# Kernel optimization log

Hardware: AMD Instinct MI355X
Metric: run time of the kernel (lower is better)

Reference implementation:

```python
import jax, jax.numpy as jnp
import numpy as np

B, K, D = 128, 32, 1024
E = 32
H = int(D * 0.25)  # d_hidden = d_block * moe_ratio


def _rsqrt_uniform(key, shape, d):
    bound = d ** -0.5
    return jax.random.uniform(key, shape, jnp.float32, -bound, bound)


def setup_inputs() -> dict:
    key = jax.random.key(0)
    ks = jax.random.split(key, 7)
    return {
        "x": jax.random.normal(ks[0], (B, K, D), jnp.float32),
        "router_w": _rsqrt_uniform(ks[1], (E, D), D),   # nn.Linear(d_block, num_experts).weight
        "router_b": _rsqrt_uniform(ks[2], (E,), D),
        "weights1": _rsqrt_uniform(ks[3], (E, D, H), H),
        "bias1": _rsqrt_uniform(ks[4], (E, H), H),
        "weights2": _rsqrt_uniform(ks[5], (E, H, D), D),
        "bias2": _rsqrt_uniform(ks[6], (E, D), D),
    }


def reference(x, router_w, router_b, weights1, bias1, weights2, bias2):
    b, k, d = x.shape
    x_flat = x.reshape(-1, d)                      # [N, D], N = B*K
    n = x_flat.shape[0]
    # top-1 router (argmax of logits, like torch.argmax)
    logits = x_flat @ router_w.T + router_b        # [N, E]
    routed_idx = jnp.argmax(logits, axis=-1)       # [N]

    # Each expert is a 2-layer MLP; note the original applies act1 (ReLU)
    # after BOTH layers, and dropout=0.0 is an identity.
    def expert_mlp(w1, b1, w2, b2):
        h = jax.nn.relu(x_flat @ w1 + b1)          # [N, H]
        return jax.nn.relu(h @ w2 + b2)            # [N, D]

    y_all = jax.vmap(expert_mlp)(weights1, bias1, weights2, bias2)  # [E, N, D]
    out_flat = y_all[routed_idx, jnp.arange(n)]    # select routed expert per token
    return out_flat.reshape(b, k, d)
```

## Files before the change

kernel.cpp:

```cpp
#include <hip/hip_runtime.h>


#define N_TOK 4096
#define DDIM  1024
#define HDIM  256
#define NEXP  32
#define TPX   136
#define NSLOT (8 * TPX)

typedef __attribute__((ext_vector_type(8))) short bf16x8;
typedef __attribute__((ext_vector_type(4))) float f32x4;

__device__ __forceinline__ unsigned short f2bf(float f) {
  union { float f; unsigned u; } v; v.f = f;
  unsigned r = v.u + 0x7FFFu + ((v.u >> 16) & 1u);
  return (unsigned short)(r >> 16);
}
__device__ __forceinline__ float bf2f(unsigned short h) {
  union { unsigned u; float f; } v; v.u = ((unsigned)h) << 16;
  return v.f;
}
__device__ __forceinline__ int swz(int row, int kk) {
  return row * 72 + (kk ^ (((row >> 3) & 7) << 3));
}

__global__ __launch_bounds__(512) void router_kernel(
    const float* __restrict__ x, const float* __restrict__ rw,
    const float* __restrict__ rb, int* __restrict__ routed) {
  __shared__ float red[8][64][8];
  int b = blockIdx.x;
  int t = threadIdx.x, w = t >> 6, l = t & 63;
  int m = l & 15, kb = l >> 4;
  int tok = b * 16 + m;
  int kbase = w * 128;
  bf16x8 wh[2][4], wl[2][4];
#pragma unroll
  for (int h = 0; h < 2; h++) {
    const float* wp = rw + (size_t)(m + h * 16) * DDIM + kbase + kb * 8;
#pragma unroll
    for (int q = 0; q < 4; q++) {
      float4 f0 = *(const float4*)(wp + q * 32);
      float4 f1 = *(const float4*)(wp + q * 32 + 4);
      float fv[8] = {f0.x, f0.y, f0.z, f0.w, f1.x, f1.y, f1.z, f1.w};
      bf16x8 hi, lo;
#pragma unroll
      for (int i = 0; i < 8; i++) {
        unsigned short hh = f2bf(fv[i]);
        hi[i] = (short)hh;
        lo[i] = (short)f2bf(fv[i] - bf2f(hh));
      }
      wh[h][q] = hi; wl[h][q] = lo;
    }
  }
  const float* xrow = x + (size_t)tok * DDIM + kbase + kb * 8;
  f32x4 acc0 = {0.f,0.f,0.f,0.f}, acc1 = {0.f,0.f,0.f,0.f};
#pragma unroll
  for (int q = 0; q < 4; q++) {
    float4 xa = *(const float4*)(xrow + q * 32);
    float4 xc = *(const float4*)(xrow + q * 32 + 4);
    float xv[8] = {xa.x, xa.y, xa.z, xa.w, xc.x, xc.y, xc.z, xc.w};
    bf16x8 xhi, xlo;
#pragma unroll
    for (int i = 0; i < 8; i++) {
      unsigned short hh = f2bf(xv[i]);
      xhi[i] = (short)hh;
      xlo[i] = (short)f2bf(xv[i] - bf2f(hh));
    }
    acc0 = __builtin_amdgcn_mfma_f32_16x16x32_bf16(xhi, wh[0][q], acc0, 0, 0, 0);
    acc0 = __builtin_amdgcn_mfma_f32_16x16x32_bf16(xlo, wh[0][q], acc0, 0, 0, 0);
    acc0 = __builtin_amdgcn_mfma_f32_16x16x32_bf16(xhi, wl[0][q], acc0, 0, 0, 0);
    acc0 = __builtin_amdgcn_mfma_f32_16x16x32_bf16(xlo, wl[0][q], acc0, 0, 0, 0);
    acc1 = __builtin_amdgcn_mfma_f32_16x16x32_bf16(xhi, wh[1][q], acc1, 0, 0, 0);
    acc1 = __builtin_amdgcn_mfma_f32_16x16x32_bf16(xlo, wh[1][q], acc1, 0, 0, 0);
    acc1 = __builtin_amdgcn_mfma_f32_16x16x32_bf16(xhi, wl[1][q], acc1, 0, 0, 0);
    acc1 = __builtin_amdgcn_mfma_f32_16x16x32_bf16(xlo, wl[1][q], acc1, 0, 0, 0);
  }
  *(f32x4*)&red[w][l][0] = acc0;
  *(f32x4*)&red[w][l][4] = acc1;
  __syncthreads();
  if (w == 0) {
    f32x4 s0 = {0.f,0.f,0.f,0.f}, s1 = {0.f,0.f,0.f,0.f};
#pragma unroll
    for (int ww = 0; ww < 8; ww++) {
      s0 += *(const f32x4*)&red[ww][l][0];
      s1 += *(const f32x4*)&red[ww][l][4];
    }
    float rb0 = rb[m], rb1 = rb[16 + m];
#pragma unroll
    for (int r = 0; r < 4; r++) {
      float v0 = s0[r] + rb0;
      float v1 = s1[r] + rb1;
      float val = v0; int idx = m;
      if (v1 > v0) { val = v1; idx = 16 + m; }
#pragma unroll
      for (int s = 1; s < 16; s <<= 1) {
        float ov = __shfl_xor(val, s);
        int oi = __shfl_xor(idx, s);
        if (ov > val || (ov == val && oi < idx)) { val = ov; idx = oi; }
      }
      if (m == 0) routed[b * 16 + kb * 4 + r] = idx;
    }
  }
}

__global__ __launch_bounds__(512) void scan_scatter_kernel(const int* __restrict__ routed,
    int* __restrict__ meta, int* __restrict__ order) {
  __shared__ int scnt[NEXP];
  __shared__ int scur[NEXP];
  int t = threadIdx.x;
  if (t < NEXP) scnt[t] = 0;
  __syncthreads();
  for (int n = t; n < N_TOK; n += 512) atomicAdd(&scnt[routed[n]], 1);
  __syncthreads();
  if (t < NEXP) {
    int c = scnt[t];
    int nt = (c + 31) >> 5;
    int ic = c;
#pragma unroll
    for (int s = 1; s < NEXP; s <<= 1) {
      int pc = __shfl_up(ic, s);
      if (t >= s) ic += pc;
    }
    int off = ic - c;
    scur[t] = off;
    int cls = t & 7, pos = t >> 3;
    int rank = 0;
#pragma unroll
    for (int j = 0; j < 4; j++) {
      int v = __shfl(nt, cls + j * 8);
      if (pos > j) rank += v;
    }
    for (int s2 = 0; s2 < nt; s2++) {
      int nr = c - s2 * 32; if (nr > 32) nr = 32;
      meta[8 + cls + 8 * (rank + s2)] = (t << 24) | (nr << 16) | (off + s2 * 32);
    }
    if (pos == 3) meta[cls] = rank + nt;
  }
  __syncthreads();
  for (int n = t; n < N_TOK; n += 512) {
    int e = routed[n];
    int p = atomicAdd(&scur[e], 1);
    order[p] = n;
  }
}

template <int KDIM, int NTOT, bool A_FP32, bool OUT_BF16>
__global__ __launch_bounds__(512) void expert_gemm_kernel(
    const void* __restrict__ a_src, const float* __restrict__ wsrc,
    const float* __restrict__ bias, const int* __restrict__ meta,
    const int* __restrict__ order, void* __restrict__ outp) {
  constexpr int NCH = KDIM / 64;
  __shared__ unsigned short AT[2][32 * 72];
  __shared__ unsigned short BT[2][128 * 72];
  int bid = blockIdx.x, xcd = bid & 7, idx = bid >> 3;
  if (idx >= meta[xcd]) return;
  int info = meta[8 + bid];
  int e = info >> 24, nrow = (info >> 16) & 0xff, ts = info & 0xffff;
  int c0 = blockIdx.y * 128;
  int t = threadIdx.x, w = t >> 6, l = t & 63, m = l & 15, kb = l >> 4;
  int atr = t >> 4, ak4 = (t & 15) * 4;
  int bcn = t & 127, bkg = t >> 7;
  int atok = order[ts + (atr < nrow ? atr : nrow - 1)];
  const float* aF = (const float*)a_src + (size_t)atok * KDIM + ak4;
  const unsigned short* aH = (const unsigned short*)a_src + (size_t)atok * KDIM + ak4;
  const float* bS = wsrc + (size_t)e * KDIM * NTOT + (size_t)(bkg * 16) * NTOT + c0 + bcn;

  float4 nAf; ushort4 nAh;
  float nB[16];
  auto LOADC = [&](int c) {
    if constexpr (A_FP32) nAf = *(const float4*)(aF + c * 64);
    else                  nAh = *(const ushort4*)(aH + c * 64);
#pragma unroll
    for (int j = 0; j < 8; j++) {
      nB[2*j]   = bS[(size_t)(c * 64 + 2*j) * NTOT];
      nB[2*j+1] = bS[(size_t)(c * 64 + 2*j + 1) * NTOT];
    }
  };

  f32x4 acc0 = {0.f,0.f,0.f,0.f}, acc1 = {0.f,0.f,0.f,0.f};
  LOADC(0);
  for (int c = 0; c < NCH; c++) {
    int p = c & 1;
    ushort4 av;
    if constexpr (A_FP32) {
      av.x = f2bf(nAf.x); av.y = f2bf(nAf.y); av.z = f2bf(nAf.z); av.w = f2bf(nAf.w);
    } else av = nAh;
    float cB[16];
#pragma unroll
    for (int j = 0; j < 16; j++) cB[j] = nB[j];
    if (c + 1 < NCH) LOADC(c + 1);
    *(ushort4*)&AT[p][swz(atr, ak4)] = av;
#pragma unroll
    for (int j = 0; j < 8; j++) {
      ushort2 pk; pk.x = f2bf(cB[2*j]); pk.y = f2bf(cB[2*j+1]);
      *(ushort2*)&BT[p][swz(bcn, bkg * 16 + 2*j)] = pk;
    }
    asm volatile("s_waitcnt lgkmcnt(0)" ::: "memory");
    __builtin_amdgcn_s_barrier();
#pragma unroll
    for (int ks = 0; ks < 2; ks++) {
      int kk = ks * 32 + kb * 8;
      bf16x8 bfr = *(const bf16x8*)&BT[p][swz(w * 16 + m, kk)];
      bf16x8 a0  = *(const bf16x8*)&AT[p][swz(m, kk)];
      bf16x8 a1  = *(const bf16x8*)&AT[p][swz(16 + m, kk)];
      acc0 = __builtin_amdgcn_mfma_f32_16x16x32_bf16(a0, bfr, acc0, 0, 0, 0);
      acc1 = __builtin_amdgcn_mfma_f32_16x16x32_bf16(a1, bfr, acc1, 0, 0, 0);
    }
  }
  int col = c0 + w * 16 + m;
  float bz = bias[e * NTOT + col];
#pragma unroll
  for (int r = 0; r < 4; r++) {
    int r0 = kb * 4 + r;
    if (r0 < nrow) {
      int tok = order[ts + r0];
      float v = acc0[r] + bz; v = v > 0.f ? v : 0.f;
      if constexpr (OUT_BF16)
        ((unsigned short*)outp)[(size_t)tok * NTOT + col] = f2bf(v);
      else
        ((float*)outp)[(size_t)tok * NTOT + col] = v;
    }
    int r1 = 16 + kb * 4 + r;
    if (r1 < nrow) {
      int tok = order[ts + r1];
      float v = acc1[r] + bz; v = v > 0.f ? v : 0.f;
      if constexpr (OUT_BF16)
        ((unsigned short*)outp)[(size_t)tok * NTOT + col] = f2bf(v);
      else
        ((float*)outp)[(size_t)tok * NTOT + col] = v;
    }
  }
}


extern "C" void kernel_launch(void* const* d_in, const int* in_sizes, int n_in,
                              void* d_out, int out_size, void* d_ws, size_t ws_size,
                              hipStream_t stream) {
  const float* x  = (const float*)d_in[0];
  const float* rw = (const float*)d_in[1];
  const float* rb = (const float*)d_in[2];
  const float* w1 = (const float*)d_in[3];
  const float* b1 = (const float*)d_in[4];
  const float* w2 = (const float*)d_in[5];
  const float* b2 = (const float*)d_in[6];
  float* out = (float*)d_out;

  char* ws = (char*)d_ws;
  unsigned short* hb = (unsigned short*)(ws + 0);
  int* routed = (int*)(ws + 2097152);
  int* order  = (int*)(ws + 2113536);
  int* meta   = (int*)(ws + 2129920);

  router_kernel<<<dim3(256), dim3(512), 0, stream>>>(x, rw, rb, routed);
  scan_scatter_kernel<<<dim3(1), dim3(512), 0, stream>>>(routed, meta, order);
  expert_gemm_kernel<DDIM, HDIM, true, true><<<dim3(NSLOT, 2), dim3(512), 0, stream>>>(
      x, w1, b1, meta, order, hb);
  expert_gemm_kernel<HDIM, DDIM, false, false><<<dim3(NSLOT, 8), dim3(512), 0, stream>>>(
      hb, w2, b2, meta, order, out);
}
```

Baseline: 62.03 us.

## Fuse scan into router via last-block counter and retile expert GEMMs to 64x64

The separate scan/scatter kernel is merged into the router kernel. The last block to finish, found with an atomic done counter reset by a memset, performs the expert histogram and scatter. The expert GEMM tiles change from 32 tokens x 128 columns with 512 threads to 64 tokens x 64 columns with 256 threads. Each wave now issues four MFMAs per B fragment, and token ids are cached in shared memory. This raises A-row reuse of each weight tile and cuts one kernel launch, at the cost of more padding waste for experts with few tokens and a serialized tail in the router.

```diff
diff --git a/kernel.cpp b/kernel.cpp
--- a/kernel.cpp
+++ b/kernel.cpp
@@ -5,7 +5,7 @@
 #define DDIM  1024
 #define HDIM  256
 #define NEXP  32
-#define TPX   136
+#define TPX   72
 #define NSLOT (8 * TPX)
 
 typedef __attribute__((ext_vector_type(8))) short bf16x8;
@@ -24,10 +24,14 @@
   return row * 72 + (kk ^ (((row >> 3) & 7) << 3));
 }
 
-__global__ __launch_bounds__(512) void router_kernel(
+__global__ __launch_bounds__(512) void router_scan_kernel(
     const float* __restrict__ x, const float* __restrict__ rw,
-    const float* __restrict__ rb, int* __restrict__ routed) {
+    const float* __restrict__ rb, int* __restrict__ routed,
+    int* __restrict__ meta, int* __restrict__ order, int* __restrict__ done) {
   __shared__ float red[8][64][8];
+  __shared__ int scnt[NEXP];
+  __shared__ int scur[NEXP];
+  __shared__ int lastflag;
   int b = blockIdx.x;
   int t = threadIdx.x, w = t >> 6, l = t & 63;
   int m = l & 15, kb = l >> 4;
@@ -101,20 +105,22 @@
       if (m == 0) routed[b * 16 + kb * 4 + r] = idx;
     }
   }
-}
-
-__global__ __launch_bounds__(512) void scan_scatter_kernel(const int* __restrict__ routed,
-    int* __restrict__ meta, int* __restrict__ order) {
-  __shared__ int scnt[NEXP];
-  __shared__ int scur[NEXP];
-  int t = threadIdx.x;
+  __syncthreads();
+  if (t == 0) {
+    __threadfence();
+    int v = atomicAdd(done, 1);
+    lastflag = (v == 255);
+    if (lastflag) __threadfence();
+  }
+  __syncthreads();
+  if (!lastflag) return;
   if (t < NEXP) scnt[t] = 0;
   __syncthreads();
   for (int n = t; n < N_TOK; n += 512) atomicAdd(&scnt[routed[n]], 1);
   __syncthreads();
   if (t < NEXP) {
     int c = scnt[t];
-    int nt = (c + 31) >> 5;
+    int nt = (c + 63) >> 6;
     int ic = c;
 #pragma unroll
     for (int s = 1; s < NEXP; s <<= 1) {
@@ -131,8 +137,8 @@
       if (pos > j) rank += v;
     }
     for (int s2 = 0; s2 < nt; s2++) {
-      int nr = c - s2 * 32; if (nr > 32) nr = 32;
-      meta[8 + cls + 8 * (rank + s2)] = (t << 24) | (nr << 16) | (off + s2 * 32);
+      int nr = c - s2 * 64; if (nr > 64) nr = 64;
+      meta[8 + cls + 8 * (rank + s2)] = (t << 24) | (nr << 16) | (off + s2 * 64);
     }
     if (pos == 3) meta[cls] = rank + nt;
   }
@@ -145,89 +151,99 @@
 }
 
 template <int KDIM, int NTOT, bool A_FP32, bool OUT_BF16>
-__global__ __launch_bounds__(512) void expert_gemm_kernel(
+__global__ __launch_bounds__(256, 4) void expert_gemm_kernel(
     const void* __restrict__ a_src, const float* __restrict__ wsrc,
     const float* __restrict__ bias, const int* __restrict__ meta,
     const int* __restrict__ order, void* __restrict__ outp) {
   constexpr int NCH = KDIM / 64;
-  __shared__ unsigned short AT[2][32 * 72];
-  __shared__ unsigned short BT[2][128 * 72];
+  __shared__ unsigned short AT[2][64 * 72];
+  __shared__ unsigned short BT[2][64 * 72];
+  __shared__ int toks[64];
   int bid = blockIdx.x, xcd = bid & 7, idx = bid >> 3;
   if (idx >= meta[xcd]) return;
   int info = meta[8 + bid];
   int e = info >> 24, nrow = (info >> 16) & 0xff, ts = info & 0xffff;
-  int c0 = blockIdx.y * 128;
+  int c0 = blockIdx.y * 64;
   int t = threadIdx.x, w = t >> 6, l = t & 63, m = l & 15, kb = l >> 4;
-  int atr = t >> 4, ak4 = (t & 15) * 4;
-  int bcn = t & 127, bkg = t >> 7;
-  int atok = order[ts + (atr < nrow ? atr : nrow - 1)];
-  const float* aF = (const float*)a_src + (size_t)atok * KDIM + ak4;
-  const unsigned short* aH = (const unsigned short*)a_src + (size_t)atok * KDIM + ak4;
-  const float* bS = wsrc + (size_t)e * KDIM * NTOT + (size_t)(bkg * 16) * NTOT + c0 + bcn;
-
-  float4 nAf; ushort4 nAh;
+  int arow = t >> 2, la = t & 3;
+  int bcn = t & 63, bkg = t >> 6;
+  int atok = order[ts + (arow < nrow ? arow : nrow - 1)];
+  if (la == 0) toks[arow] = atok;
+  const float* aF = (const float*)a_src + (size_t)atok * KDIM;
+  const unsigned short* aH = (const unsigned short*)a_src + (size_t)atok * KDIM;
+  const float* bS = wsrc + (size_t)e * KDIM * NTOT + c0 + bcn;
+
+  float4 nAf[4]; bf16x8 nAh[2];
   float nB[16];
   auto LOADC = [&](int c) {
-    if constexpr (A_FP32) nAf = *(const float4*)(aF + c * 64);
-    else                  nAh = *(const ushort4*)(aH + c * 64);
-#pragma unroll
-    for (int j = 0; j < 8; j++) {
-      nB[2*j]   = bS[(size_t)(c * 64 + 2*j) * NTOT];
-      nB[2*j+1] = bS[(size_t)(c * 64 + 2*j + 1) * NTOT];
-    }
+    if constexpr (A_FP32) {
+#pragma unroll
+      for (int j = 0; j < 4; j++)
+        nAf[j] = *(const float4*)(aF + c * 64 + la * 4 + j * 16);
+    } else {
+#pragma unroll
+      for (int j = 0; j < 2; j++)
+        nAh[j] = *(const bf16x8*)(aH + c * 64 + la * 8 + j * 32);
+    }
+#pragma unroll
+    for (int jj = 0; jj < 16; jj++)
+      nB[jj] = bS[(size_t)(c * 64 + bkg * 16 + jj) * NTOT];
   };
 
-  f32x4 acc0 = {0.f,0.f,0.f,0.f}, acc1 = {0.f,0.f,0.f,0.f};
+  f32x4 acc[4];
+#pragma unroll
+  for (int rt = 0; rt < 4; rt++) acc[rt] = (f32x4){0.f,0.f,0.f,0.f};
   LOADC(0);
   for (int c = 0; c < NCH; c++) {
     int p = c & 1;
-    ushort4 av;
     if constexpr (A_FP32) {
-      av.x = f2bf(nAf.x); av.y = f2bf(nAf.y); av.z = f2bf(nAf.z); av.w = f2bf(nAf.w);
-    } else av = nAh;
-    float cB[16];
-#pragma unroll
-    for (int j = 0; j < 16; j++) cB[j] = nB[j];
+#pragma unroll
+      for (int j = 0; j < 4; j++) {
+        ushort4 av;
+        av.x = f2bf(nAf[j].x); av.y = f2bf(nAf[j].y);
+        av.z = f2bf(nAf[j].z); av.w = f2bf(nAf[j].w);
+        *(ushort4*)&AT[p][swz(arow, la * 4 + j * 16)] = av;
+      }
+    } else {
+#pragma unroll
+      for (int j = 0; j < 2; j++)
+        *(bf16x8*)&AT[p][swz(arow, la * 8 + j * 32)] = nAh[j];
+    }
+#pragma unroll
+    for (int j = 0; j < 4; j++) {
+      ushort4 pv;
+      pv.x = f2bf(nB[4*j]);   pv.y = f2bf(nB[4*j+1]);
+      pv.z = f2bf(nB[4*j+2]); pv.w = f2bf(nB[4*j+3]);
+      *(ushort4*)&BT[p][swz(bcn, bkg * 16 + 4 * j)] = pv;
+    }
     if (c + 1 < NCH) LOADC(c + 1);
-    *(ushort4*)&AT[p][swz(atr, ak4)] = av;
-#pragma unroll
-    for (int j = 0; j < 8; j++) {
-      ushort2 pk; pk.x = f2bf(cB[2*j]); pk.y = f2bf(cB[2*j+1]);
-      *(ushort2*)&BT[p][swz(bcn, bkg * 16 + 2*j)] = pk;
-    }
     asm volatile("s_waitcnt lgkmcnt(0)" ::: "memory");
     __builtin_amdgcn_s_barrier();
 #pragma unroll
     for (int ks = 0; ks < 2; ks++) {
       int kk = ks * 32 + kb * 8;
       bf16x8 bfr = *(const bf16x8*)&BT[p][swz(w * 16 + m, kk)];
-      bf16x8 a0  = *(const bf16x8*)&AT[p][swz(m, kk)];
-      bf16x8 a1  = *(const bf16x8*)&AT[p][swz(16 + m, kk)];
-      acc0 = __builtin_amdgcn_mfma_f32_16x16x32_bf16(a0, bfr, acc0, 0, 0, 0);
-      acc1 = __builtin_amdgcn_mfma_f32_16x16x32_bf16(a1, bfr, acc1, 0, 0, 0);
+#pragma unroll
+      for (int rt = 0; rt < 4; rt++) {
+        bf16x8 av = *(const bf16x8*)&AT[p][swz(rt * 16 + m, kk)];
+        acc[rt] = __builtin_amdgcn_mfma_f32_16x16x32_bf16(av, bfr, acc[rt], 0, 0, 0);
+      }
     }
   }
   int col = c0 + w * 16 + m;
   float bz = bias[e * NTOT + col];
 #pragma unroll
-  for (int r = 0; r < 4; r++) {
-    int r0 = kb * 4 + r;
-    if (r0 < nrow) {
-      int tok = order[ts + r0];
-      float v = acc0[r] + bz; v = v > 0.f ? v : 0.f;
-      if constexpr (OUT_BF16)
-        ((unsigned short*)outp)[(size_t)tok * NTOT + col] = f2bf(v);
-      else
-        ((float*)outp)[(size_t)tok * NTOT + col] = v;
-    }
-    int r1 = 16 + kb * 4 + r;
-    if (r1 < nrow) {
-      int tok = order[ts + r1];
-      float v = acc1[r] + bz; v = v > 0.f ? v : 0.f;
-      if constexpr (OUT_BF16)
-        ((unsigned short*)outp)[(size_t)tok * NTOT + col] = f2bf(v);
-      else
-        ((float*)outp)[(size_t)tok * NTOT + col] = v;
+  for (int rt = 0; rt < 4; rt++) {
+#pragma unroll
+    for (int r = 0; r < 4; r++) {
+      int rl = rt * 16 + kb * 4 + r;
+      if (rl < nrow) {
+        float v = acc[rt][r] + bz; v = v > 0.f ? v : 0.f;
+        if constexpr (OUT_BF16)
+          ((unsigned short*)outp)[(size_t)toks[rl] * NTOT + col] = f2bf(v);
+        else
+          ((float*)outp)[(size_t)toks[rl] * NTOT + col] = v;
+      }
     }
   }
 }
@@ -250,11 +266,13 @@
   int* routed = (int*)(ws + 2097152);
   int* order  = (int*)(ws + 2113536);
   int* meta   = (int*)(ws + 2129920);
-
-  router_kernel<<<dim3(256), dim3(512), 0, stream>>>(x, rw, rb, routed);
-  scan_scatter_kernel<<<dim3(1), dim3(512), 0, stream>>>(routed, meta, order);
-  expert_gemm_kernel<DDIM, HDIM, true, true><<<dim3(NSLOT, 2), dim3(512), 0, stream>>>(
+  int* done   = (int*)(ws + 2133504);
+
+  hipMemsetAsync(done, 0, 4, stream);
+  router_scan_kernel<<<dim3(256), dim3(512), 0, stream>>>(
+      x, rw, rb, routed, meta, order, done);
+  expert_gemm_kernel<DDIM, HDIM, true, true><<<dim3(NSLOT, 4), dim3(256), 0, stream>>>(
       x, w1, b1, meta, order, hb);
-  expert_gemm_kernel<HDIM, DDIM, false, false><<<dim3(NSLOT, 8), dim3(512), 0, stream>>>(
+  expert_gemm_kernel<HDIM, DDIM, false, false><<<dim3(NSLOT, 16), dim3(256), 0, stream>>>(
       hb, w2, b2, meta, order, out);
 }
```

Result: slower. 73.07 us (+17.8%).
